# Kernel tuning notes

Hardware: AMD Instinct MI355X
Metric: run time of the kernel (lower is better)

The kernel has to match this reference:

```python
import jax, jax.numpy as jnp
import numpy as np

INPUT_DIM = 256
OUTPUT_DIM = 512
NUM_KNOTS = 64
RANGE_KNOTS = (-1.0, 1.0)
DEGREE = 3
BATCH = 4096


def bspline_basis(x, knots, degree):
    """Cox-de Boor recursion. x: [B, I], knots: [K] (uniform, ascending).
    Returns basis values [B, I, K - degree - 1]."""
    xe = x[..., None]  # [B, I, 1]
    # degree-0: indicator of knot interval k, k = 0..K-2
    basis = ((xe >= knots[:-1]) & (xe < knots[1:])).astype(x.dtype)  # [B, I, K-1]
    for d in range(1, degree + 1):
        k = np.arange(knots.shape[0] - d - 1)
        left = (xe - knots[k]) / (knots[k + d] - knots[k]) * basis[..., :-1]
        right = (knots[k + d + 1] - xe) / (knots[k + d + 1] - knots[k + 1]) * basis[..., 1:]
        basis = left + right  # [B, I, K-d-1]
    return basis


def setup_inputs() -> dict:
    key = jax.random.key(0)
    kx, kb, ks = jax.random.split(key, 3)
    x = jax.random.uniform(kx, (BATCH, INPUT_DIM), dtype=jnp.float32)
    wb = jax.random.uniform(kb, (INPUT_DIM, OUTPUT_DIM), dtype=jnp.float32)
    ws = jax.random.uniform(ks, (INPUT_DIM, OUTPUT_DIM), dtype=jnp.float32)
    cps = jnp.ones((INPUT_DIM, NUM_KNOTS), dtype=jnp.float32)
    knots = jnp.asarray(np.linspace(RANGE_KNOTS[0], RANGE_KNOTS[1], NUM_KNOTS), dtype=jnp.float32)
    return {"x": x, "wb": wb, "ws": ws, "cps": cps, "knots": knots}


def reference(x, wb, ws, cps, knots):
    num_basis = NUM_KNOTS - DEGREE - 1
    basis = bspline_basis(x, knots, DEGREE)            # [B, I, num_basis]
    # per-input-dim spline value: sum_k cps[i, k] * B_k(x[b, i])
    spline = jnp.einsum('bik,ik->bi', basis, cps[:, :num_basis])  # [B, I]
    base = jax.nn.silu(x)                               # [B, I]
    # out[b, o] = sum_i wb[i, o] * silu(x[b, i]) + ws[i, o] * spline[b, i]
    out = base @ wb + spline @ ws                       # [B, O]
    return out
```

## Files before the change

### kernel.cpp

```cpp
#include <hip/hip_runtime.h>
#include <hip/hip_bf16.h>

#define BATCH    4096
#define IN_DIM   256
#define OUT_DIM  512
#define KDIM     512
#define NKNOTS   64
#define NBASIS   60

typedef __attribute__((ext_vector_type(8))) short bf16x8;
typedef __attribute__((ext_vector_type(4))) float f32x4;

__device__ __align__(16) short g_A [BATCH   * KDIM];
__device__ __align__(16) short g_Bt[OUT_DIM * KDIM];

__device__ __forceinline__ short f2bf(float f) {
    __hip_bfloat16 h = __float2bfloat16(f);
    return *reinterpret_cast<short*>(&h);
}

#define NBLK_A 512
#define NBLK_B 64

__global__ __launch_bounds__(256) void prep_kernel(
        const float* __restrict__ x, const float* __restrict__ wb,
        const float* __restrict__ ws, const float* __restrict__ cps) {
    __shared__ float T[64][65];

    if (blockIdx.x < NBLK_A) {
        const int g  = blockIdx.x * 256 + threadIdx.x;
        const int b  = g >> 5;
        const int i0 = (g & 31) << 3;
        float xv[8];
        *(f32x4*)&xv[0] = *(const f32x4*)&x[b * IN_DIM + i0];
        *(f32x4*)&xv[4] = *(const f32x4*)&x[b * IN_DIM + i0 + 4];
        bf16x8 sil, spl;
        #pragma unroll
        for (int e = 0; e < 8; ++e) {
            float v = xv[e];
            float s = v / (1.0f + __expf(-v));
            float u  = (v + 1.0f) * 31.5f;
            float fj = floorf(u);
            int   j  = (int)fj;
            float sp = 0.0f;
            if (j >= 0 && j <= 62) {
                float t  = u - fj;
                float t2 = t * t, t3 = t2 * t;
                float omt = 1.0f - t;
                const float c6 = 1.0f / 6.0f;
                float w0 = omt * omt * omt * c6;
                float w1 = (3.0f*t3 - 6.0f*t2 + 4.0f) * c6;
                float w2 = (-3.0f*t3 + 3.0f*t2 + 3.0f*t + 1.0f) * c6;
                float w3 = t3 * c6;
                const float* cp = cps + (i0 + e) * NKNOTS;
                int k0 = j - 3;
                if (k0     >= 0 && k0     < NBASIS) sp += w0 * cp[k0];
                if (k0 + 1 >= 0 && k0 + 1 < NBASIS) sp += w1 * cp[k0 + 1];
                if (k0 + 2 >= 0 && k0 + 2 < NBASIS) sp += w2 * cp[k0 + 2];
                if (               k0 + 3 < NBASIS) sp += w3 * cp[k0 + 3];
            }
            sil[e] = f2bf(s);
            spl[e] = f2bf(sp);
        }
        *(bf16x8*)&g_A[b * KDIM + i0]          = sil;
        *(bf16x8*)&g_A[b * KDIM + IN_DIM + i0] = spl;
    } else {
        const int bb = blockIdx.x - NBLK_A;
        const int k0 = (bb >> 3) * 64;
        const int n0 = (bb & 7) * 64;
        const float* W = (k0 < IN_DIM) ? wb + (size_t)k0 * OUT_DIM
                                       : ws + (size_t)(k0 - IN_DIM) * OUT_DIM;
        const int t  = threadIdx.x;
        const int r  = t >> 2;
        const int c0 = (t & 3) * 16;
        #pragma unroll
        for (int e = 0; e < 16; e += 4) {
            f32x4 v = *(const f32x4*)&W[r * OUT_DIM + n0 + c0 + e];
            T[r][c0 + e + 0] = v[0];
            T[r][c0 + e + 1] = v[1];
            T[r][c0 + e + 2] = v[2];
            T[r][c0 + e + 3] = v[3];
        }
        __syncthreads();
        short tmp[16];
        #pragma unroll
        for (int e = 0; e < 16; ++e) tmp[e] = f2bf(T[c0 + e][r]);
        *(bf16x8*)&g_Bt[(n0 + r) * KDIM + k0 + c0]     = *(bf16x8*)&tmp[0];
        *(bf16x8*)&g_Bt[(n0 + r) * KDIM + k0 + c0 + 8] = *(bf16x8*)&tmp[8];
    }
}

#define BM 64
#define BN 64
#define BK 128
#define LDSS 136

__global__ __launch_bounds__(256) void gemm_kernel(float* __restrict__ C) {
    __shared__ __align__(16) short As[BM * LDSS];
    __shared__ __align__(16) short Bs[BN * LDSS];

    const int bid  = blockIdx.x;
    const int sbid = (bid & 7) * 64 + (bid >> 3);
    const int m0   = (sbid >> 3) * 64;
    const int n0   = (sbid & 7) * 64;
    const int tid  = threadIdx.x;
    const int lane = tid & 63;
    const int wave = tid >> 6;
    const int wm   = (wave & 1) * 32;
    const int wn   = (wave >> 1) * 32;
    const int fr   = lane & 15;
    const int koff = (lane >> 4) * 8;

    f32x4 acc[2][2] = {};

    for (int k0 = 0; k0 < KDIM; k0 += BK) {
        #pragma unroll
        for (int s = 0; s < 4; ++s) {
            const int c = tid + s * 256;
            const int r = c >> 4, o = (c & 15) * 8;
            *(uint4*)&As[r * LDSS + o] = *(const uint4*)&g_A [(m0 + r) * KDIM + k0 + o];
            *(uint4*)&Bs[r * LDSS + o] = *(const uint4*)&g_Bt[(n0 + r) * KDIM + k0 + o];
        }
        __syncthreads();

        #pragma unroll
        for (int kk = 0; kk < BK; kk += 32) {
            bf16x8 a0 = *(const bf16x8*)&As[(wm + fr)      * LDSS + kk + koff];
            bf16x8 a1 = *(const bf16x8*)&As[(wm + 16 + fr) * LDSS + kk + koff];
            bf16x8 b0 = *(const bf16x8*)&Bs[(wn + fr)      * LDSS + kk + koff];
            bf16x8 b1 = *(const bf16x8*)&Bs[(wn + 16 + fr) * LDSS + kk + koff];
            acc[0][0] = __builtin_amdgcn_mfma_f32_16x16x32_bf16(a0, b0, acc[0][0], 0, 0, 0);
            acc[0][1] = __builtin_amdgcn_mfma_f32_16x16x32_bf16(a0, b1, acc[0][1], 0, 0, 0);
            acc[1][0] = __builtin_amdgcn_mfma_f32_16x16x32_bf16(a1, b0, acc[1][0], 0, 0, 0);
            acc[1][1] = __builtin_amdgcn_mfma_f32_16x16x32_bf16(a1, b1, acc[1][1], 0, 0, 0);
        }
        __syncthreads();
    }

    const int rbase = (lane >> 4) * 4;
    #pragma unroll
    for (int mt = 0; mt < 2; ++mt) {
        #pragma unroll
        for (int nt = 0; nt < 2; ++nt) {
            #pragma unroll
            for (int r = 0; r < 4; ++r) {
                int row = m0 + wm + mt * 16 + rbase + r;
                int col = n0 + wn + nt * 16 + fr;
                C[row * OUT_DIM + col] = acc[mt][nt][r];
            }
        }
    }
}

extern "C" void kernel_launch(void* const* d_in, const int* in_sizes, int n_in,
                              void* d_out, int out_size, void* d_ws, size_t ws_size,
                              hipStream_t stream) {
    (void)in_sizes; (void)n_in; (void)d_ws; (void)ws_size; (void)out_size;
    const float* x   = (const float*)d_in[0];
    const float* wb  = (const float*)d_in[1];
    const float* wsp = (const float*)d_in[2];
    const float* cps = (const float*)d_in[3];
    float* out = (float*)d_out;

    prep_kernel<<<NBLK_A + NBLK_B, 256, 0, stream>>>(x, wb, wsp, cps);
    gemm_kernel<<<512, 256, 0, stream>>>(out);
}
```

Before: 78.04 us.

## Double-buffer GEMM LDS tiles with register prefetch and merge prep blocks

The GEMM kernel now uses two LDS buffers and prefetches the next K tile into registers while MFMAs run on the current tile, so each step needs one barrier instead of two. The prep kernel folds the weight transpose work into the first 64 activation blocks, which shrinks the grid from 576 to 512 blocks. The prefetch costs extra registers and twice the LDS per block, and the first 64 prep blocks now do more work than the rest.

```diff
diff --git a/kernel.cpp b/kernel.cpp
--- a/kernel.cpp
+++ b/kernel.cpp
@@ -19,15 +19,14 @@
     return *reinterpret_cast<short*>(&h);
 }
 
-#define NBLK_A 512
-#define NBLK_B 64
+#define NBLK_PREP 512
 
 __global__ __launch_bounds__(256) void prep_kernel(
         const float* __restrict__ x, const float* __restrict__ wb,
         const float* __restrict__ ws, const float* __restrict__ cps) {
     __shared__ float T[64][65];
 
-    if (blockIdx.x < NBLK_A) {
+    {
         const int g  = blockIdx.x * 256 + threadIdx.x;
         const int b  = g >> 5;
         const int i0 = (g & 31) << 3;
@@ -64,8 +63,10 @@
         }
         *(bf16x8*)&g_A[b * KDIM + i0]          = sil;
         *(bf16x8*)&g_A[b * KDIM + IN_DIM + i0] = spl;
-    } else {
-        const int bb = blockIdx.x - NBLK_A;
+    }
+
+    if (blockIdx.x < 64) {
+        const int bb = blockIdx.x;
         const int k0 = (bb >> 3) * 64;
         const int n0 = (bb & 7) * 64;
         const float* W = (k0 < IN_DIM) ? wb + (size_t)k0 * OUT_DIM
@@ -96,8 +97,8 @@
 #define LDSS 136
 
 __global__ __launch_bounds__(256) void gemm_kernel(float* __restrict__ C) {
-    __shared__ __align__(16) short As[BM * LDSS];
-    __shared__ __align__(16) short Bs[BN * LDSS];
+    __shared__ __align__(16) short As[2][BM * LDSS];
+    __shared__ __align__(16) short Bs[2][BN * LDSS];
 
     const int bid  = blockIdx.x;
     const int sbid = (bid & 7) * 64 + (bid >> 3);
@@ -111,30 +112,61 @@
     const int fr   = lane & 15;
     const int koff = (lane >> 4) * 8;
 
+    const int r_st = tid >> 4;
+    const int o_st = (tid & 15) * 8;
+
+    uint4 ra[4], rb[4];
+    #pragma unroll
+    for (int s = 0; s < 4; ++s) {
+        const int r = r_st + s * 16;
+        ra[s] = *(const uint4*)&g_A [(m0 + r) * KDIM + o_st];
+        rb[s] = *(const uint4*)&g_Bt[(n0 + r) * KDIM + o_st];
+    }
+    #pragma unroll
+    for (int s = 0; s < 4; ++s) {
+        const int r = r_st + s * 16;
+        *(uint4*)&As[0][r * LDSS + o_st] = ra[s];
+        *(uint4*)&Bs[0][r * LDSS + o_st] = rb[s];
+    }
+    __syncthreads();
+
     f32x4 acc[2][2] = {};
 
-    for (int k0 = 0; k0 < KDIM; k0 += BK) {
-        #pragma unroll
-        for (int s = 0; s < 4; ++s) {
-            const int c = tid + s * 256;
-            const int r = c >> 4, o = (c & 15) * 8;
-            *(uint4*)&As[r * LDSS + o] = *(const uint4*)&g_A [(m0 + r) * KDIM + k0 + o];
-            *(uint4*)&Bs[r * LDSS + o] = *(const uint4*)&g_Bt[(n0 + r) * KDIM + k0 + o];
+    #pragma unroll
+    for (int t = 0; t < 4; ++t) {
+        const int cur = t & 1;
+        if (t < 3) {
+            const int k0 = (t + 1) * BK;
+            #pragma unroll
+            for (int s = 0; s < 4; ++s) {
+                const int r = r_st + s * 16;
+                ra[s] = *(const uint4*)&g_A [(m0 + r) * KDIM + k0 + o_st];
+                rb[s] = *(const uint4*)&g_Bt[(n0 + r) * KDIM + k0 + o_st];
+            }
         }
-        __syncthreads();
 
         #pragma unroll
         for (int kk = 0; kk < BK; kk += 32) {
-            bf16x8 a0 = *(const bf16x8*)&As[(wm + fr)      * LDSS + kk + koff];
-            bf16x8 a1 = *(const bf16x8*)&As[(wm + 16 + fr) * LDSS + kk + koff];
-            bf16x8 b0 = *(const bf16x8*)&Bs[(wn + fr)      * LDSS + kk + koff];
-            bf16x8 b1 = *(const bf16x8*)&Bs[(wn + 16 + fr) * LDSS + kk + koff];
+            bf16x8 a0 = *(const bf16x8*)&As[cur][(wm + fr)      * LDSS + kk + koff];
+            bf16x8 a1 = *(const bf16x8*)&As[cur][(wm + 16 + fr) * LDSS + kk + koff];
+            bf16x8 b0 = *(const bf16x8*)&Bs[cur][(wn + fr)      * LDSS + kk + koff];
+            bf16x8 b1 = *(const bf16x8*)&Bs[cur][(wn + 16 + fr) * LDSS + kk + koff];
             acc[0][0] = __builtin_amdgcn_mfma_f32_16x16x32_bf16(a0, b0, acc[0][0], 0, 0, 0);
             acc[0][1] = __builtin_amdgcn_mfma_f32_16x16x32_bf16(a0, b1, acc[0][1], 0, 0, 0);
             acc[1][0] = __builtin_amdgcn_mfma_f32_16x16x32_bf16(a1, b0, acc[1][0], 0, 0, 0);
             acc[1][1] = __builtin_amdgcn_mfma_f32_16x16x32_bf16(a1, b1, acc[1][1], 0, 0, 0);
         }
-        __syncthreads();
+
+        if (t < 3) {
+            const int nxt = cur ^ 1;
+            #pragma unroll
+            for (int s = 0; s < 4; ++s) {
+                const int r = r_st + s * 16;
+                *(uint4*)&As[nxt][r * LDSS + o_st] = ra[s];
+                *(uint4*)&Bs[nxt][r * LDSS + o_st] = rb[s];
+            }
+            __syncthreads();
+        }
     }
 
     const int rbase = (lane >> 4) * 4;
@@ -162,6 +194,6 @@
     const float* cps = (const float*)d_in[3];
     float* out = (float*)d_out;
 
-    prep_kernel<<<NBLK_A + NBLK_B, 256, 0, stream>>>(x, wb, wsp, cps);
+    prep_kernel<<<NBLK_PREP, 256, 0, stream>>>(x, wb, wsp, cps);
     gemm_kernel<<<512, 256, 0, stream>>>(out);
 }
```

Result: no change. 79.06 us (+1.3%).
